# Kernel optimization log

Hardware: AMD Instinct MI355X
Metric: run time of the kernel (lower is better)

## Reference

```python
import jax, jax.numpy as jnp
import numpy as np

N = 100000        # points
C_IN = 64         # in_planes
C_OUT = 64        # out_planes (== mid_planes)
SHARE = 8         # share_planes
NS = 16           # nsample
CW = C_OUT // SHARE  # attention channels (8)
EPS = 1e-5


def _bn(x, gamma, beta):
    # PointBatchNorm in training mode: normalize over all axes except channel (last)
    ax = tuple(range(x.ndim - 1))
    m = jnp.mean(x, axis=ax)
    v = jnp.var(x, axis=ax)
    return gamma * (x - m) * jax.lax.rsqrt(v + EPS) + beta


def setup_inputs() -> dict:
    key = jax.random.key(0)
    ks = jax.random.split(key, 20)
    s = 0.05
    inp = {
        "p": jax.random.normal(ks[0], (N, 3), jnp.float32) * 5.0,
        "x": jax.random.normal(ks[1], (N, C_IN), jnp.float32),
        "o": jnp.array([N], jnp.int32),
        "idx": jax.random.randint(ks[2], (N, NS), 0, N, jnp.int32),
        # q/k/v linears
        "Wq": jax.random.normal(ks[3], (C_IN, C_OUT), jnp.float32) * s,
        "bq": jnp.zeros((C_OUT,), jnp.float32),
        "Wk": jax.random.normal(ks[4], (C_IN, C_OUT), jnp.float32) * s,
        "bk": jnp.zeros((C_OUT,), jnp.float32),
        "Wv": jax.random.normal(ks[5], (C_IN, C_OUT), jnp.float32) * s,
        "bv": jnp.zeros((C_OUT,), jnp.float32),
        # linear_p: Linear(3,3) -> BN(3) -> ReLU -> Linear(3,out)
        "Wp1": jax.random.normal(ks[6], (3, 3), jnp.float32) * 0.5,
        "bp1": jnp.zeros((3,), jnp.float32),
        "gp": jnp.ones((3,), jnp.float32),
        "betap": jnp.zeros((3,), jnp.float32),
        "Wp2": jax.random.normal(ks[7], (3, C_OUT), jnp.float32) * s,
        "bp2": jnp.zeros((C_OUT,), jnp.float32),
        # linear_w: BN(mid)->ReLU->Linear(mid, CW)->BN(CW)->ReLU->Linear(CW, CW)
        "gw1": jnp.ones((C_OUT,), jnp.float32),
        "bw1": jnp.zeros((C_OUT,), jnp.float32),
        "Ww1": jax.random.normal(ks[8], (C_OUT, CW), jnp.float32) * s,
        "bww1": jnp.zeros((CW,), jnp.float32),
        "gw2": jnp.ones((CW,), jnp.float32),
        "bw2": jnp.zeros((CW,), jnp.float32),
        "Ww2": jax.random.normal(ks[9], (CW, CW), jnp.float32) * s,
        "bww2": jnp.zeros((CW,), jnp.float32),
    }
    return inp


def reference(p, x, o, idx,
              Wq, bq, Wk, bk, Wv, bv,
              Wp1, bp1, gp, betap, Wp2, bp2,
              gw1, bw1, Ww1, bww1, gw2, bw2, Ww2, bww2):
    relu = jax.nn.relu
    x_q = x @ Wq + bq                       # [n, mid]
    x_k = x @ Wk + bk                       # [n, mid]
    x_v = x @ Wv + bv                       # [n, out]
    # knn_query_and_group: gather neighbors (idx precomputed), with relative xyz
    p_r0 = p[idx] - p[:, None, :]           # [n, ns, 3]
    xk_g = x_k[idx]                         # [n, ns, mid]
    xv_g = x_v[idx]                         # [n, ns, out]
    # linear_p
    p_r = relu(_bn(p_r0 @ Wp1 + bp1, gp, betap)) @ Wp2 + bp2   # [n, ns, out]
    # einops.reduce 'n ns (i j) -> n ns j' with j=mid_planes: i==1 -> identity
    r_qk = xk_g - x_q[:, None, :] + p_r     # [n, ns, mid]
    # linear_w
    w = relu(_bn(r_qk, gw1, bw1)) @ Ww1 + bww1          # [n, ns, CW]
    w = relu(_bn(w, gw2, bw2)) @ Ww2 + bww2             # [n, ns, CW]
    w = jax.nn.softmax(w, axis=1)                        # softmax over neighbors
    # shared-channel weighted sum
    v = (xv_g + p_r).reshape(N, NS, SHARE, CW)           # [n, ns, s, i]
    out = jnp.einsum('ntsi,nti->nsi', v, w)              # [n, s, i]
    return out.reshape(N, C_OUT)
```

## Files before the change

kernel.cpp:

```cpp
#include <hip/hip_runtime.h>
#include <math.h>

#define NPTS 100000
#define NSAMP 16
#define NROWS (NPTS*NSAMP)
#define EPS 1e-5f

#define NQKV ((NPTS + 63)/64)
#define GRID_B 1024
#define GRID_C 2048
#define GRID_D 2048
#define GRID_E 2048

#define S_BN1A 0
#define S_BN1B 4
#define S_BN2A 8
#define S_BN2B 72
#define S_BN3A 136
#define S_BN3B 144
#define S_PARTB 160
#define S_PARTC (S_PARTB + GRID_B*8)
#define S_PARTD (S_PARTC + GRID_C*128)

__device__ __forceinline__ unsigned short f2bf(float f) {
    unsigned int x = __float_as_uint(f);
    unsigned int r = (x + 0x7fffu + ((x >> 16) & 1u)) >> 16;
    return (unsigned short)r;
}
__device__ __forceinline__ float bf2f(unsigned short u) {
    return __uint_as_float(((unsigned int)u) << 16);
}

typedef _Float16 h2v __attribute__((ext_vector_type(2)));
__device__ __forceinline__ float dot2u(unsigned int a, unsigned int b, float c) {
#if __has_builtin(__builtin_amdgcn_fdot2)
    return __builtin_amdgcn_fdot2(__builtin_bit_cast(h2v, a),
                                  __builtin_bit_cast(h2v, b), c, false);
#else
    h2v x = __builtin_bit_cast(h2v, a), y = __builtin_bit_cast(h2v, b);
    return c + (float)x.x*(float)y.x + (float)x.y*(float)y.y;
#endif
}

__global__ __launch_bounds__(256) void qkv_bn1_kernel(
    const float* __restrict__ x,
    const float* __restrict__ Wq, const float* __restrict__ bq,
    const float* __restrict__ Wk, const float* __restrict__ bk,
    const float* __restrict__ Wv, const float* __restrict__ bv,
    float* __restrict__ xq, unsigned short* __restrict__ xkb,
    unsigned short* __restrict__ xvb,
    const float* __restrict__ p, const int* __restrict__ idx,
    const float* __restrict__ Wp1, const float* __restrict__ bp1,
    float* __restrict__ part)
{
    __shared__ __align__(16) float xsh[64][68];
    __shared__ __align__(16) float wsh[64][64];
    __shared__ float red16[4][6];
    const int tid = threadIdx.x;

    if (blockIdx.x >= NQKV) {
        const int b = blockIdx.x - NQKV;
        float w9[9], bb[3];
        #pragma unroll
        for (int i = 0; i < 9; ++i) w9[i] = Wp1[i];
        #pragma unroll
        for (int i = 0; i < 3; ++i) bb[i] = bp1[i];

        float s0=0.f,s1=0.f,s2=0.f,q0=0.f,q1=0.f,q2=0.f;
        for (int row = b*256 + tid; row < NROWS; row += GRID_B*256) {
            const int n = row >> 4;
            const int j = idx[row];
            const float d0 = p[j*3+0] - p[n*3+0];
            const float d1 = p[j*3+1] - p[n*3+1];
            const float d2 = p[j*3+2] - p[n*3+2];
            const float t0 = d0*w9[0] + d1*w9[3] + d2*w9[6] + bb[0];
            const float t1 = d0*w9[1] + d1*w9[4] + d2*w9[7] + bb[1];
            const float t2 = d0*w9[2] + d1*w9[5] + d2*w9[8] + bb[2];
            s0 += t0; s1 += t1; s2 += t2;
            q0 += t0*t0; q1 += t1*t1; q2 += t2*t2;
        }
        #pragma unroll
        for (int m = 32; m >= 1; m >>= 1) {
            s0 += __shfl_xor(s0, m); s1 += __shfl_xor(s1, m); s2 += __shfl_xor(s2, m);
            q0 += __shfl_xor(q0, m); q1 += __shfl_xor(q1, m); q2 += __shfl_xor(q2, m);
        }
        const int lane = tid & 63, wid = tid >> 6;
        if (lane == 0) {
            red16[wid][0]=s0; red16[wid][1]=s1; red16[wid][2]=s2;
            red16[wid][3]=q0; red16[wid][4]=q1; red16[wid][5]=q2;
        }
        __syncthreads();
        if (tid < 6)
            part[b*8 + tid] = red16[0][tid]+red16[1][tid]+red16[2][tid]+red16[3][tid];
        return;
    }

    const int r0 = blockIdx.x * 64;
    {
        const int row = tid >> 4, c4 = tid & 15;
        #pragma unroll
        for (int rr = 0; rr < 4; ++rr) {
            const int r = row + rr*16;
            const int gr = r0 + r;
            float4 v = (gr < NPTS) ? *(const float4*)&x[(size_t)gr*64 + c4*4]
                                   : make_float4(0.f, 0.f, 0.f, 0.f);
            *(float4*)&xsh[r][c4*4] = v;
        }
    }

    const int tr = tid >> 4, tc = tid & 15;

    for (int m = 0; m < 3; ++m) {
        const float* __restrict__ W  = (m == 0) ? Wq : (m == 1) ? Wk : Wv;
        const float* __restrict__ bs = (m == 0) ? bq : (m == 1) ? bk : bv;

        __syncthreads();
        for (int l = tid; l < 1024; l += 256)
            *(float4*)&wsh[l >> 4][(l & 15)*4] = *(const float4*)&W[l*4];
        __syncthreads();

        float acc[4][4];
        {
            const float4 b4 = *(const float4*)&bs[tc*4];
            #pragma unroll
            for (int rr = 0; rr < 4; ++rr) {
                acc[rr][0] = b4.x; acc[rr][1] = b4.y;
                acc[rr][2] = b4.z; acc[rr][3] = b4.w;
            }
        }

        #pragma unroll 4
        for (int k4 = 0; k4 < 16; ++k4) {
            float4 xr[4];
            #pragma unroll
            for (int rr = 0; rr < 4; ++rr)
                xr[rr] = *(const float4*)&xsh[tr + 16*rr][k4*4];
            float4 wr[4];
            #pragma unroll
            for (int kk = 0; kk < 4; ++kk)
                wr[kk] = *(const float4*)&wsh[k4*4 + kk][tc*4];
            #pragma unroll
            for (int rr = 0; rr < 4; ++rr) {
                acc[rr][0] += xr[rr].x*wr[0].x + xr[rr].y*wr[1].x + xr[rr].z*wr[2].x + xr[rr].w*wr[3].x;
                acc[rr][1] += xr[rr].x*wr[0].y + xr[rr].y*wr[1].y + xr[rr].z*wr[2].y + xr[rr].w*wr[3].y;
                acc[rr][2] += xr[rr].x*wr[0].z + xr[rr].y*wr[1].z + xr[rr].z*wr[2].z + xr[rr].w*wr[3].z;
                acc[rr][3] += xr[rr].x*wr[0].w + xr[rr].y*wr[1].w + xr[rr].z*wr[2].w + xr[rr].w*wr[3].w;
            }
        }

        #pragma unroll
        for (int rr = 0; rr < 4; ++rr) {
            const int gr = r0 + tr + 16*rr;
            if (gr < NPTS) {
                if (m == 0) {
                    float4 o;
                    o.x = acc[rr][0]; o.y = acc[rr][1]; o.z = acc[rr][2]; o.w = acc[rr][3];
                    *(float4*)&xq[(size_t)gr*64 + tc*4] = o;
                } else {
                    unsigned short* dst = (m == 1) ? xkb : xvb;
                    ushort4 o;
                    o.x = f2bf(acc[rr][0]); o.y = f2bf(acc[rr][1]);
                    o.z = f2bf(acc[rr][2]); o.w = f2bf(acc[rr][3]);
                    *(ushort4*)&dst[(size_t)gr*64 + tc*4] = o;
                }
            }
        }
    }
}

__global__ __launch_bounds__(256) void bn_fin_kernel(
    const float* __restrict__ part, int nblk, int stride, int nch,
    const float* __restrict__ g, const float* __restrict__ beta,
    float* __restrict__ aout, float* __restrict__ bout)
{
    const int c = blockIdx.x;
    const int tid = threadIdx.x;
    float s = 0.f, q = 0.f;
    for (int b = tid; b < nblk; b += 256) {
        s += part[(size_t)b*stride + c];
        q += part[(size_t)b*stride + nch + c];
    }
    #pragma unroll
    for (int m = 32; m >= 1; m >>= 1) { s += __shfl_xor(s, m); q += __shfl_xor(q, m); }
    __shared__ float rs[4], rq[4];
    if ((tid & 63) == 0) { rs[tid >> 6] = s; rq[tid >> 6] = q; }
    __syncthreads();
    if (tid == 0) {
        s = rs[0]+rs[1]+rs[2]+rs[3];
        q = rq[0]+rq[1]+rq[2]+rq[3];
        const float inv = 1.0f / (float)NROWS;
        const float mean = s * inv;
        const float var = fmaxf(q * inv - mean*mean, 0.f);
        const float a = g[c] * rsqrtf(var + EPS);
        aout[c] = a;
        bout[c] = beta[c] - a * mean;
    }
}

__global__ __launch_bounds__(256, 8) void bn2_stats_kernel(
    const float* __restrict__ p, const int* __restrict__ idx,
    const float* __restrict__ xq, const unsigned short* __restrict__ xkb,
    const float* __restrict__ Wp1, const float* __restrict__ bp1,
    const float* __restrict__ Wp2, const float* __restrict__ bp2,
    const float* __restrict__ st, float* __restrict__ part)
{
    __shared__ float4 hjs[4][16];
    const int tid = threadIdx.x, lane = tid & 63, wid = tid >> 6;
    float w9[9], bb[3], a1[3], b1[3];
    #pragma unroll
    for (int i = 0; i < 9; ++i) w9[i] = Wp1[i];
    #pragma unroll
    for (int i = 0; i < 3; ++i) { bb[i] = bp1[i]; a1[i] = st[S_BN1A+i]; b1[i] = st[S_BN1B+i]; }
    const float wc0 = Wp2[lane], wc1 = Wp2[64+lane], wc2 = Wp2[128+lane], bpc = bp2[lane];

    float s = 0.f, q = 0.f;
    const int nw = gridDim.x * 4;
    for (int pt = blockIdx.x*4 + wid; pt < NPTS; pt += nw) {
        const float xqc = xq[(size_t)pt*64 + lane];
        if (lane < 16) {
            const int j = idx[pt*16 + lane];
            const float pn0 = p[pt*3], pn1 = p[pt*3+1], pn2 = p[pt*3+2];
            const float d0 = p[j*3] - pn0, d1 = p[j*3+1] - pn1, d2 = p[j*3+2] - pn2;
            const float t0 = d0*w9[0] + d1*w9[3] + d2*w9[6] + bb[0];
            const float t1 = d0*w9[1] + d1*w9[4] + d2*w9[7] + bb[1];
            const float t2 = d0*w9[2] + d1*w9[5] + d2*w9[8] + bb[2];
            float4 h;
            h.x = fmaxf(a1[0]*t0 + b1[0], 0.f);
            h.y = fmaxf(a1[1]*t1 + b1[1], 0.f);
            h.z = fmaxf(a1[2]*t2 + b1[2], 0.f);
            h.w = __int_as_float(j);
            hjs[wid][lane] = h;
        }
        #pragma unroll
        for (int t = 0; t < 16; ++t) {
            const float4 hv = hjs[wid][t];
            const int j = __float_as_int(hv.w);
            const float pr = hv.x*wc0 + hv.y*wc1 + hv.z*wc2 + bpc;
            const float r = bf2f(xkb[(size_t)j*64 + lane]) - xqc + pr;
            s += r; q += r*r;
        }
    }
    __shared__ float redS[4][64], redQ[4][64];
    redS[wid][lane] = s; redQ[wid][lane] = q;
    __syncthreads();
    if (tid < 64) {
        const float S = redS[0][tid]+redS[1][tid]+redS[2][tid]+redS[3][tid];
        const float Q = redQ[0][tid]+redQ[1][tid]+redQ[2][tid]+redQ[3][tid];
        part[(size_t)blockIdx.x*128 + tid] = S;
        part[(size_t)blockIdx.x*128 + 64 + tid] = Q;
    }
}

__global__ __launch_bounds__(256, 8) void w1_kernel(
    const float* __restrict__ p, const int* __restrict__ idx,
    const float* __restrict__ xq, const unsigned short* __restrict__ xkb,
    const float* __restrict__ Wp1, const float* __restrict__ bp1,
    const float* __restrict__ Wp2, const float* __restrict__ bp2,
    const float* __restrict__ Ww1, const float* __restrict__ bww1,
    const float* __restrict__ st, unsigned short* __restrict__ w1out,
    float* __restrict__ part)
{
    __shared__ float4 hjs[4][16];
    __shared__ __align__(16) unsigned int hl6[4][16][36];
    __shared__ __align__(16) unsigned int wT6[8][36];
    const int tid = threadIdx.x, lane = tid & 63, wid = tid >> 6;

    for (int l = tid; l < 512; l += 256) {
        const int c = l >> 3, j = l & 7;
        ((_Float16*)&wT6[j][0])[c] = (_Float16)Ww1[l];
    }
    __syncthreads();

    float w9[9], bb[3], a1[3], b1[3];
    #pragma unroll
    for (int i = 0; i < 9; ++i) w9[i] = Wp1[i];
    #pragma unroll
    for (int i = 0; i < 3; ++i) { bb[i] = bp1[i]; a1[i] = st[S_BN1A+i]; b1[i] = st[S_BN1B+i]; }

    const int c = lane;
    const float wc0 = Wp2[c], wc1 = Wp2[64+c], wc2 = Wp2[128+c], bpc = bp2[c];
    const float a2c = st[S_BN2A + c], b2c = st[S_BN2B + c];
    const int j8 = lane & 7, tt = lane >> 3;
    const float bw1j = bww1[j8];

    float s3 = 0.f, q3 = 0.f;
    const int nw = gridDim.x * 4;
    for (int pt = blockIdx.x*4 + wid; pt < NPTS; pt += nw) {
        const float xqc = xq[(size_t)pt*64 + lane];
        if (lane < 16) {
            const int j = idx[pt*16 + lane];
            const float pn0 = p[pt*3], pn1 = p[pt*3+1], pn2 = p[pt*3+2];
            const float d0 = p[j*3] - pn0, d1 = p[j*3+1] - pn1, d2 = p[j*3+2] - pn2;
            const float t0v = d0*w9[0] + d1*w9[3] + d2*w9[6] + bb[0];
            const float t1v = d0*w9[1] + d1*w9[4] + d2*w9[7] + bb[1];
            const float t2v = d0*w9[2] + d1*w9[5] + d2*w9[8] + bb[2];
            float4 h;
            h.x = fmaxf(a1[0]*t0v + b1[0], 0.f);
            h.y = fmaxf(a1[1]*t1v + b1[1], 0.f);
            h.z = fmaxf(a1[2]*t2v + b1[2], 0.f);
            h.w = __int_as_float(j);
            hjs[wid][lane] = h;
        }
        #pragma unroll
        for (int t = 0; t < 16; ++t) {
            const float4 hv = hjs[wid][t];
            const int j = __float_as_int(hv.w);
            const float pr = hv.x*wc0 + hv.y*wc1 + hv.z*wc2 + bpc;
            const float r = bf2f(xkb[(size_t)j*64 + lane]) - xqc + pr;
            ((_Float16*)&hl6[wid][t][0])[lane] = (_Float16)fmaxf(a2c*r + b2c, 0.f);
        }

        float acc0 = bw1j, acc1 = bw1j;
        const uint4* hA = (const uint4*)&hl6[wid][tt][0];
        const uint4* hB = (const uint4*)&hl6[wid][tt + 8][0];
        const uint4* wp = (const uint4*)&wT6[j8][0];
        #pragma unroll
        for (int k = 0; k < 8; ++k) {
            const uint4 w4 = wp[k];
            const uint4 a4 = hA[k];
            const uint4 b4 = hB[k];
            acc0 = dot2u(a4.x, w4.x, acc0); acc1 = dot2u(b4.x, w4.x, acc1);
            acc0 = dot2u(a4.y, w4.y, acc0); acc1 = dot2u(b4.y, w4.y, acc1);
            acc0 = dot2u(a4.z, w4.z, acc0); acc1 = dot2u(b4.z, w4.z, acc1);
            acc0 = dot2u(a4.w, w4.w, acc0); acc1 = dot2u(b4.w, w4.w, acc1);
        }
        w1out[(size_t)pt*128 + lane]      = f2bf(acc0);
        w1out[(size_t)pt*128 + 64 + lane] = f2bf(acc1);
        s3 += acc0 + acc1;
        q3 += acc0*acc0 + acc1*acc1;
    }

    s3 += __shfl_xor(s3, 8);  q3 += __shfl_xor(q3, 8);
    s3 += __shfl_xor(s3, 16); q3 += __shfl_xor(q3, 16);
    s3 += __shfl_xor(s3, 32); q3 += __shfl_xor(q3, 32);
    __shared__ float redS[4][8], redQ[4][8];
    if (lane < 8) { redS[wid][lane] = s3; redQ[wid][lane] = q3; }
    __syncthreads();
    if (tid < 8) {
        const float S = redS[0][tid]+redS[1][tid]+redS[2][tid]+redS[3][tid];
        const float Q = redQ[0][tid]+redQ[1][tid]+redQ[2][tid]+redQ[3][tid];
        part[(size_t)blockIdx.x*16 + tid]     = S;
        part[(size_t)blockIdx.x*16 + 8 + tid] = Q;
    }
}

__global__ __launch_bounds__(256, 8) void out_kernel(
    const float* __restrict__ p, const int* __restrict__ idx,
    const unsigned short* __restrict__ xvb, const unsigned short* __restrict__ w1b,
    const float* __restrict__ Wp1, const float* __restrict__ bp1,
    const float* __restrict__ Wp2, const float* __restrict__ bp2,
    const float* __restrict__ Ww2, const float* __restrict__ bww2,
    const float* __restrict__ st, float* __restrict__ out)
{
    __shared__ float4 hjs[4][16];
    __shared__ float wl[4][16][8];
    const int tid = threadIdx.x, lane = tid & 63, wid = tid >> 6;
    const int j8 = lane & 7, t0 = lane >> 3;

    float w9[9], bb[3], a1[3], b1[3];
    #pragma unroll
    for (int i = 0; i < 9; ++i) w9[i] = Wp1[i];
    #pragma unroll
    for (int i = 0; i < 3; ++i) { bb[i] = bp1[i]; a1[i] = st[S_BN1A+i]; b1[i] = st[S_BN1B+i]; }
    float ww2c[8];
    #pragma unroll
    for (int i = 0; i < 8; ++i) ww2c[i] = Ww2[i*8 + j8];
    const float a3j = st[S_BN3A + j8], b3j = st[S_BN3B + j8];
    const float bw2j = bww2[j8];
    const int c = lane;
    const float wc0 = Wp2[c], wc1 = Wp2[64+c], wc2 = Wp2[128+c], bpc = bp2[c];

    const int nw = gridDim.x * 4;
    for (int pt = blockIdx.x*4 + wid; pt < NPTS; pt += nw) {
        if (lane < 16) {
            const int j = idx[pt*16 + lane];
            const float pn0 = p[pt*3], pn1 = p[pt*3+1], pn2 = p[pt*3+2];
            const float d0 = p[j*3] - pn0, d1 = p[j*3+1] - pn1, d2 = p[j*3+2] - pn2;
            const float t1v = d0*w9[0] + d1*w9[3] + d2*w9[6] + bb[0];
            const float t2v = d0*w9[1] + d1*w9[4] + d2*w9[7] + bb[1];
            const float t3v = d0*w9[2] + d1*w9[5] + d2*w9[8] + bb[2];
            float4 h;
            h.x = fmaxf(a1[0]*t1v + b1[0], 0.f);
            h.y = fmaxf(a1[1]*t2v + b1[1], 0.f);
            h.z = fmaxf(a1[2]*t3v + b1[2], 0.f);
            h.w = __int_as_float(j);
            hjs[wid][lane] = h;
        }

        const float val0 = bf2f(w1b[(size_t)pt*128 + lane]);
        const float val1 = bf2f(w1b[(size_t)pt*128 + 64 + lane]);
        const float r0 = fmaxf(a3j*val0 + b3j, 0.f);
        const float r1 = fmaxf(a3j*val1 + b3j, 0.f);
        float v0 = bw2j, v1 = bw2j;
        const int gbase = lane & 56;
        #pragma unroll
        for (int jj = 0; jj < 8; ++jj) {
            v0 += __shfl(r0, gbase + jj) * ww2c[jj];
            v1 += __shfl(r1, gbase + jj) * ww2c[jj];
        }

        float m = fmaxf(v0, v1);
        m = fmaxf(m, __shfl_xor(m, 8));
        m = fmaxf(m, __shfl_xor(m, 16));
        m = fmaxf(m, __shfl_xor(m, 32));
        float e0 = __expf(v0 - m), e1 = __expf(v1 - m);
        float ssum = e0 + e1;
        ssum += __shfl_xor(ssum, 8);
        ssum += __shfl_xor(ssum, 16);
        ssum += __shfl_xor(ssum, 32);
        const float inv = 1.0f / ssum;
        wl[wid][t0][j8]     = e0 * inv;
        wl[wid][t0 + 8][j8] = e1 * inv;

        float acc = 0.f;
        #pragma unroll
        for (int t = 0; t < 16; ++t) {
            const float4 hv = hjs[wid][t];
            const int j = __float_as_int(hv.w);
            const float pr = hv.x*wc0 + hv.y*wc1 + hv.z*wc2 + bpc;
            const float wt = wl[wid][t][j8];
            acc += (bf2f(xvb[(size_t)j*64 + c]) + pr) * wt;
        }
        out[(size_t)pt*64 + c] = acc;
    }
}

extern "C" void kernel_launch(void* const* d_in, const int* in_sizes, int n_in,
                              void* d_out, int out_size, void* d_ws, size_t ws_size,
                              hipStream_t stream)
{
    const float* p    = (const float*)d_in[0];
    const float* x    = (const float*)d_in[1];
    const int*   idx  = (const int*)d_in[3];
    const float* Wq   = (const float*)d_in[4];
    const float* bq   = (const float*)d_in[5];
    const float* Wk   = (const float*)d_in[6];
    const float* bk   = (const float*)d_in[7];
    const float* Wv   = (const float*)d_in[8];
    const float* bv   = (const float*)d_in[9];
    const float* Wp1  = (const float*)d_in[10];
    const float* bp1  = (const float*)d_in[11];
    const float* gp   = (const float*)d_in[12];
    const float* betap= (const float*)d_in[13];
    const float* Wp2  = (const float*)d_in[14];
    const float* bp2  = (const float*)d_in[15];
    const float* gw1  = (const float*)d_in[16];
    const float* bw1  = (const float*)d_in[17];
    const float* Ww1  = (const float*)d_in[18];
    const float* bww1 = (const float*)d_in[19];
    const float* gw2  = (const float*)d_in[20];
    const float* bw2  = (const float*)d_in[21];
    const float* Ww2  = (const float*)d_in[22];
    const float* bww2 = (const float*)d_in[23];

    float* out = (float*)d_out;
    float* ws  = (float*)d_ws;

    float*          xq  = ws;
    unsigned short* xkb = (unsigned short*)(ws + (size_t)NPTS*64);
    unsigned short* xvb = (unsigned short*)(ws + (size_t)NPTS*96);
    unsigned short* w1b = (unsigned short*)(ws + (size_t)NPTS*128);
    float*          st  = ws + (size_t)NPTS*192;

    qkv_bn1_kernel<<<NQKV + GRID_B, 256, 0, stream>>>(
        x, Wq, bq, Wk, bk, Wv, bv, xq, xkb, xvb,
        p, idx, Wp1, bp1, st + S_PARTB);
    bn_fin_kernel<<<3, 256, 0, stream>>>(st + S_PARTB, GRID_B, 8, 3, gp, betap,
                                         st + S_BN1A, st + S_BN1B);

    bn2_stats_kernel<<<GRID_C, 256, 0, stream>>>(p, idx, xq, xkb, Wp1, bp1, Wp2, bp2,
                                                 st, st + S_PARTC);
    bn_fin_kernel<<<64, 256, 0, stream>>>(st + S_PARTC, GRID_C, 128, 64, gw1, bw1,
                                          st + S_BN2A, st + S_BN2B);

    w1_kernel<<<GRID_D, 256, 0, stream>>>(p, idx, xq, xkb, Wp1, bp1, Wp2, bp2,
                                          Ww1, bww1, st, w1b, st + S_PARTD);
    bn_fin_kernel<<<8, 256, 0, stream>>>(st + S_PARTD, GRID_D, 16, 8, gw2, bw2,
                                         st + S_BN3A, st + S_BN3B);

    out_kernel<<<GRID_E, 256, 0, stream>>>(p, idx, xvb, w1b, Wp1, bp1, Wp2, bp2,
                                           Ww2, bww2, st, out);
}
```

Baseline: 265.0 us.

## Use MFMA bf16 for W1 projection and readlane broadcast of neighbor data

The per-neighbor relative-position features and neighbor indices are now computed redundantly in every lane and broadcast with readlane, replacing the LDS staging array in three kernels. This removes LDS round trips and the divergent lane<16 branch. The 64x8 linear_w first layer is moved from fp16 dot2 on LDS data to two bf16 MFMA 16x16x32 instructions, using an XOR-swizzled LDS tile. Precision changes from fp16 to bf16 for that matmul, which adds rounding error.

Result: faster. 251.5 us (-5.1%).

```diff
diff --git a/kernel.cpp b/kernel.cpp
--- a/kernel.cpp
+++ b/kernel.cpp
@@ -22,6 +22,9 @@
 #define S_PARTC (S_PARTB + GRID_B*8)
 #define S_PARTD (S_PARTC + GRID_C*128)
 
+typedef __attribute__((ext_vector_type(8))) short bf16x8;
+typedef __attribute__((ext_vector_type(4))) float f32x4;
+
 __device__ __forceinline__ unsigned short f2bf(float f) {
     unsigned int x = __float_as_uint(f);
     unsigned int r = (x + 0x7fffu + ((x >> 16) & 1u)) >> 16;
@@ -30,16 +33,8 @@
 __device__ __forceinline__ float bf2f(unsigned short u) {
     return __uint_as_float(((unsigned int)u) << 16);
 }
-
-typedef _Float16 h2v __attribute__((ext_vector_type(2)));
-__device__ __forceinline__ float dot2u(unsigned int a, unsigned int b, float c) {
-#if __has_builtin(__builtin_amdgcn_fdot2)
-    return __builtin_amdgcn_fdot2(__builtin_bit_cast(h2v, a),
-                                  __builtin_bit_cast(h2v, b), c, false);
-#else
-    h2v x = __builtin_bit_cast(h2v, a), y = __builtin_bit_cast(h2v, b);
-    return c + (float)x.x*(float)y.x + (float)x.y*(float)y.y;
-#endif
+__device__ __forceinline__ float rlF(float v, int t) {
+    return __int_as_float(__builtin_amdgcn_readlane(__float_as_int(v), t));
 }
 
 __global__ __launch_bounds__(256) void qkv_bn1_kernel(
@@ -204,7 +199,6 @@
     const float* __restrict__ Wp2, const float* __restrict__ bp2,
     const float* __restrict__ st, float* __restrict__ part)
 {
-    __shared__ float4 hjs[4][16];
     const int tid = threadIdx.x, lane = tid & 63, wid = tid >> 6;
     float w9[9], bb[3], a1[3], b1[3];
     #pragma unroll
@@ -212,32 +206,29 @@
     #pragma unroll
     for (int i = 0; i < 3; ++i) { bb[i] = bp1[i]; a1[i] = st[S_BN1A+i]; b1[i] = st[S_BN1B+i]; }
     const float wc0 = Wp2[lane], wc1 = Wp2[64+lane], wc2 = Wp2[128+lane], bpc = bp2[lane];
+    const int lane16 = lane & 15;
 
     float s = 0.f, q = 0.f;
     const int nw = gridDim.x * 4;
     for (int pt = blockIdx.x*4 + wid; pt < NPTS; pt += nw) {
         const float xqc = xq[(size_t)pt*64 + lane];
-        if (lane < 16) {
-            const int j = idx[pt*16 + lane];
-            const float pn0 = p[pt*3], pn1 = p[pt*3+1], pn2 = p[pt*3+2];
-            const float d0 = p[j*3] - pn0, d1 = p[j*3+1] - pn1, d2 = p[j*3+2] - pn2;
-            const float t0 = d0*w9[0] + d1*w9[3] + d2*w9[6] + bb[0];
-            const float t1 = d0*w9[1] + d1*w9[4] + d2*w9[7] + bb[1];
-            const float t2 = d0*w9[2] + d1*w9[5] + d2*w9[8] + bb[2];
-            float4 h;
-            h.x = fmaxf(a1[0]*t0 + b1[0], 0.f);
-            h.y = fmaxf(a1[1]*t1 + b1[1], 0.f);
-            h.z = fmaxf(a1[2]*t2 + b1[2], 0.f);
-            h.w = __int_as_float(j);
-            hjs[wid][lane] = h;
-        }
+        const int jreg = idx[pt*16 + lane16];
+        const float pn0 = p[pt*3], pn1 = p[pt*3+1], pn2 = p[pt*3+2];
+        const float d0 = p[jreg*3] - pn0, d1 = p[jreg*3+1] - pn1, d2 = p[jreg*3+2] - pn2;
+        const float t0 = d0*w9[0] + d1*w9[3] + d2*w9[6] + bb[0];
+        const float t1 = d0*w9[1] + d1*w9[4] + d2*w9[7] + bb[1];
+        const float t2 = d0*w9[2] + d1*w9[5] + d2*w9[8] + bb[2];
+        const float h0 = fmaxf(a1[0]*t0 + b1[0], 0.f);
+        const float h1 = fmaxf(a1[1]*t1 + b1[1], 0.f);
+        const float h2 = fmaxf(a1[2]*t2 + b1[2], 0.f);
+
         #pragma unroll
         for (int t = 0; t < 16; ++t) {
-            const float4 hv = hjs[wid][t];
-            const int j = __float_as_int(hv.w);
-            const float pr = hv.x*wc0 + hv.y*wc1 + hv.z*wc2 + bpc;
-            const float r = bf2f(xkb[(size_t)j*64 + lane]) - xqc + pr;
-            s += r; q += r*r;
+            const int jt = __builtin_amdgcn_readlane(jreg, t);
+            const float g0 = rlF(h0, t), g1 = rlF(h1, t), g2 = rlF(h2, t);
+            const float pr = fmaf(g0, wc0, fmaf(g1, wc1, fmaf(g2, wc2, bpc)));
+            const float r = bf2f(xkb[(size_t)jt*64 + lane]) - xqc + pr;
+            s += r; q = fmaf(r, r, q);
         }
     }
     __shared__ float redS[4][64], redQ[4][64];
@@ -260,16 +251,8 @@
     const float* __restrict__ st, unsigned short* __restrict__ w1out,
     float* __restrict__ part)
 {
-    __shared__ float4 hjs[4][16];
-    __shared__ __align__(16) unsigned int hl6[4][16][36];
-    __shared__ __align__(16) unsigned int wT6[8][36];
+    __shared__ unsigned short hl[4][16][64];
     const int tid = threadIdx.x, lane = tid & 63, wid = tid >> 6;
-
-    for (int l = tid; l < 512; l += 256) {
-        const int c = l >> 3, j = l & 7;
-        ((_Float16*)&wT6[j][0])[c] = (_Float16)Ww1[l];
-    }
-    __syncthreads();
 
     float w9[9], bb[3], a1[3], b1[3];
     #pragma unroll
@@ -280,61 +263,87 @@
     const int c = lane;
     const float wc0 = Wp2[c], wc1 = Wp2[64+c], wc2 = Wp2[128+c], bpc = bp2[c];
     const float a2c = st[S_BN2A + c], b2c = st[S_BN2B + c];
-    const int j8 = lane & 7, tt = lane >> 3;
-    const float bw1j = bww1[j8];
-
-    float s3 = 0.f, q3 = 0.f;
+    const int lane16 = lane & 15;
+    const int kgrp = lane >> 4;
+
+    bf16x8 aF0, aF1;
+    {
+        const int m = lane16;
+        #pragma unroll
+        for (int i = 0; i < 8; ++i) {
+            const int k0 = kgrp*4 + (i & 3) + 16*(i >> 2);
+            const int i0 = (m < 8) ? (k0*8 + m) : 0;
+            const int i1 = (m < 8) ? ((k0 + 32)*8 + m) : 0;
+            aF0[i] = (m < 8) ? (short)f2bf(Ww1[i0]) : (short)0;
+            aF1[i] = (m < 8) ? (short)f2bf(Ww1[i1]) : (short)0;
+        }
+    }
+    f32x4 cb;
+    #pragma unroll
+    for (int r = 0; r < 4; ++r) cb[r] = bww1[(kgrp*4 + r) & 7];
+
+    float s3[4] = {0.f,0.f,0.f,0.f}, q3[4] = {0.f,0.f,0.f,0.f};
     const int nw = gridDim.x * 4;
     for (int pt = blockIdx.x*4 + wid; pt < NPTS; pt += nw) {
         const float xqc = xq[(size_t)pt*64 + lane];
-        if (lane < 16) {
-            const int j = idx[pt*16 + lane];
-            const float pn0 = p[pt*3], pn1 = p[pt*3+1], pn2 = p[pt*3+2];
-            const float d0 = p[j*3] - pn0, d1 = p[j*3+1] - pn1, d2 = p[j*3+2] - pn2;
-            const float t0v = d0*w9[0] + d1*w9[3] + d2*w9[6] + bb[0];
-            const float t1v = d0*w9[1] + d1*w9[4] + d2*w9[7] + bb[1];
-            const float t2v = d0*w9[2] + d1*w9[5] + d2*w9[8] + bb[2];
-            float4 h;
-            h.x = fmaxf(a1[0]*t0v + b1[0], 0.f);
-            h.y = fmaxf(a1[1]*t1v + b1[1], 0.f);
-            h.z = fmaxf(a1[2]*t2v + b1[2], 0.f);
-            h.w = __int_as_float(j);
-            hjs[wid][lane] = h;
-        }
+        const int jreg = idx[pt*16 + lane16];
+        const float pn0 = p[pt*3], pn1 = p[pt*3+1], pn2 = p[pt*3+2];
+        const float d0 = p[jreg*3] - pn0, d1 = p[jreg*3+1] - pn1, d2 = p[jreg*3+2] - pn2;
+        const float t0v = d0*w9[0] + d1*w9[3] + d2*w9[6] + bb[0];
+        const float t1v = d0*w9[1] + d1*w9[4] + d2*w9[7] + bb[1];
+        const float t2v = d0*w9[2] + d1*w9[5] + d2*w9[8] + bb[2];
+        const float h0 = fmaxf(a1[0]*t0v + b1[0], 0.f);
+        const float h1 = fmaxf(a1[1]*t1v + b1[1], 0.f);
+        const float h2 = fmaxf(a1[2]*t2v + b1[2], 0.f);
+
         #pragma unroll
         for (int t = 0; t < 16; ++t) {
-            const float4 hv = hjs[wid][t];
-            const int j = __float_as_int(hv.w);
-            const float pr = hv.x*wc0 + hv.y*wc1 + hv.z*wc2 + bpc;
-            const float r = bf2f(xkb[(size_t)j*64 + lane]) - xqc + pr;
-            ((_Float16*)&hl6[wid][t][0])[lane] = (_Float16)fmaxf(a2c*r + b2c, 0.f);
-        }
-
-        float acc0 = bw1j, acc1 = bw1j;
-        const uint4* hA = (const uint4*)&hl6[wid][tt][0];
-        const uint4* hB = (const uint4*)&hl6[wid][tt + 8][0];
-        const uint4* wp = (const uint4*)&wT6[j8][0];
-        #pragma unroll
-        for (int k = 0; k < 8; ++k) {
-            const uint4 w4 = wp[k];
-            const uint4 a4 = hA[k];
-            const uint4 b4 = hB[k];
-            acc0 = dot2u(a4.x, w4.x, acc0); acc1 = dot2u(b4.x, w4.x, acc1);
-            acc0 = dot2u(a4.y, w4.y, acc0); acc1 = dot2u(b4.y, w4.y, acc1);
-            acc0 = dot2u(a4.z, w4.z, acc0); acc1 = dot2u(b4.z, w4.z, acc1);
-            acc0 = dot2u(a4.w, w4.w, acc0); acc1 = dot2u(b4.w, w4.w, acc1);
-        }
-        w1out[(size_t)pt*128 + lane]      = f2bf(acc0);
-        w1out[(size_t)pt*128 + 64 + lane] = f2bf(acc1);
-        s3 += acc0 + acc1;
-        q3 += acc0*acc0 + acc1*acc1;
-    }
-
-    s3 += __shfl_xor(s3, 8);  q3 += __shfl_xor(q3, 8);
-    s3 += __shfl_xor(s3, 16); q3 += __shfl_xor(q3, 16);
-    s3 += __shfl_xor(s3, 32); q3 += __shfl_xor(q3, 32);
+            const int jt = __builtin_amdgcn_readlane(jreg, t);
+            const float g0 = rlF(h0, t), g1 = rlF(h1, t), g2 = rlF(h2, t);
+            const float pr = fmaf(g0, wc0, fmaf(g1, wc1, fmaf(g2, wc2, bpc)));
+            const float r = bf2f(xkb[(size_t)jt*64 + lane]) - xqc + pr;
+            const float hv = fmaxf(fmaf(a2c, r, b2c), 0.f);
+            hl[wid][t][lane ^ ((t & 7) << 3)] = f2bf(hv);
+        }
+
+        const int t = lane16;
+        const int key = (t & 7) << 3;
+        union { bf16x8 v; uint2 u[2]; } b0u, b1u;
+        b0u.u[0] = *(const uint2*)&hl[wid][t][(kgrp*4)      ^ key];
+        b0u.u[1] = *(const uint2*)&hl[wid][t][(kgrp*4 + 16) ^ key];
+        b1u.u[0] = *(const uint2*)&hl[wid][t][(kgrp*4 + 32) ^ key];
+        b1u.u[1] = *(const uint2*)&hl[wid][t][(kgrp*4 + 48) ^ key];
+
+        f32x4 acc = __builtin_amdgcn_mfma_f32_16x16x32_bf16(aF0, b0u.v, cb, 0, 0, 0);
+        acc = __builtin_amdgcn_mfma_f32_16x16x32_bf16(aF1, b1u.v, acc, 0, 0, 0);
+
+        if (lane < 32) {
+            ushort4 o;
+            o.x = f2bf(acc[0]); o.y = f2bf(acc[1]);
+            o.z = f2bf(acc[2]); o.w = f2bf(acc[3]);
+            *(ushort4*)&w1out[(size_t)pt*128 + lane16*8 + kgrp*4] = o;
+            #pragma unroll
+            for (int r = 0; r < 4; ++r) {
+                s3[r] += acc[r];
+                q3[r] = fmaf(acc[r], acc[r], q3[r]);
+            }
+        }
+    }
+
+    #pragma unroll
+    for (int m = 8; m >= 1; m >>= 1) {
+        #pragma unroll
+        for (int r = 0; r < 4; ++r) {
+            s3[r] += __shfl_xor(s3[r], m);
+            q3[r] += __shfl_xor(q3[r], m);
+        }
+    }
     __shared__ float redS[4][8], redQ[4][8];
-    if (lane < 8) { redS[wid][lane] = s3; redQ[wid][lane] = q3; }
+    if (lane == 0 || lane == 16) {
+        const int jb = (lane >> 4) * 4;
+        #pragma unroll
+        for (int r = 0; r < 4; ++r) { redS[wid][jb+r] = s3[r]; redQ[wid][jb+r] = q3[r]; }
+    }
     __syncthreads();
     if (tid < 8) {
         const float S = redS[0][tid]+redS[1][tid]+redS[2][tid]+redS[3][tid];
@@ -352,10 +361,10 @@
     const float* __restrict__ Ww2, const float* __restrict__ bww2,
     const float* __restrict__ st, float* __restrict__ out)
 {
-    __shared__ float4 hjs[4][16];
     __shared__ float wl[4][16][8];
     const int tid = threadIdx.x, lane = tid & 63, wid = tid >> 6;
     const int j8 = lane & 7, t0 = lane >> 3;
+    const int lane16 = lane & 15;
 
     float w9[9], bb[3], a1[3], b1[3];
     #pragma unroll
@@ -372,20 +381,15 @@
 
     const int nw = gridDim.x * 4;
     for (int pt = blockIdx.x*4 + wid; pt < NPTS; pt += nw) {
-        if (lane < 16) {
-            const int j = idx[pt*16 + lane];
-            const float pn0 = p[pt*3], pn1 = p[pt*3+1], pn2 = p[pt*3+2];
-            const float d0 = p[j*3] - pn0, d1 = p[j*3+1] - pn1, d2 = p[j*3+2] - pn2;
-            const float t1v = d0*w9[0] + d1*w9[3] + d2*w9[6] + bb[0];
-            const float t2v = d0*w9[1] + d1*w9[4] + d2*w9[7] + bb[1];
-            const float t3v = d0*w9[2] + d1*w9[5] + d2*w9[8] + bb[2];
-            float4 h;
-            h.x = fmaxf(a1[0]*t1v + b1[0], 0.f);
-            h.y = fmaxf(a1[1]*t2v + b1[1], 0.f);
-            h.z = fmaxf(a1[2]*t3v + b1[2], 0.f);
-            h.w = __int_as_float(j);
-            hjs[wid][lane] = h;
-        }
+        const int jreg = idx[pt*16 + lane16];
+        const float pn0 = p[pt*3], pn1 = p[pt*3+1], pn2 = p[pt*3+2];
+        const float d0 = p[jreg*3] - pn0, d1 = p[jreg*3+1] - pn1, d2 = p[jreg*3+2] - pn2;
+        const float t1v = d0*w9[0] + d1*w9[3] + d2*w9[6] + bb[0];
+        const float t2v = d0*w9[1] + d1*w9[4] + d2*w9[7] + bb[1];
+        const float t3v = d0*w9[2] + d1*w9[5] + d2*w9[8] + bb[2];
+        const float h0 = fmaxf(a1[0]*t1v + b1[0], 0.f);
+        const float h1 = fmaxf(a1[1]*t2v + b1[1], 0.f);
+        const float h2 = fmaxf(a1[2]*t3v + b1[2], 0.f);
 
         const float val0 = bf2f(w1b[(size_t)pt*128 + lane]);
         const float val1 = bf2f(w1b[(size_t)pt*128 + 64 + lane]);
@@ -415,11 +419,11 @@
         float acc = 0.f;
         #pragma unroll
         for (int t = 0; t < 16; ++t) {
-            const float4 hv = hjs[wid][t];
-            const int j = __float_as_int(hv.w);
-            const float pr = hv.x*wc0 + hv.y*wc1 + hv.z*wc2 + bpc;
+            const int jt = __builtin_amdgcn_readlane(jreg, t);
+            const float g0 = rlF(h0, t), g1 = rlF(h1, t), g2 = rlF(h2, t);
+            const float pr = fmaf(g0, wc0, fmaf(g1, wc1, fmaf(g2, wc2, bpc)));
             const float wt = wl[wid][t][j8];
-            acc += (bf2f(xvb[(size_t)j*64 + c]) + pr) * wt;
+            acc = fmaf(bf2f(xvb[(size_t)jt*64 + c]) + pr, wt, acc);
         }
         out[(size_t)pt*64 + c] = acc;
     }
```
